# Optimization experiments

Measured on AMD Instinct MI355X. Metric: run time of the kernel, lower is better.

The kernel has to match this reference:

```python
import jax, jax.numpy as jnp
import numpy as np

C = 64   # in_channels
KS = 3   # kernel_size


def _wconv(p, W1, b1, W2, b2, W3, b3):
    # 1x1 conv stack: 3 -> 64 -> 256 -> C*KS*KS, ReLU between
    h = jax.nn.relu(jnp.einsum('oc,bchw->bohw', W1, p) + b1[None, :, None, None])
    h = jax.nn.relu(jnp.einsum('oc,bchw->bohw', W2, h) + b2[None, :, None, None])
    h = jnp.einsum('oc,bchw->bohw', W3, h) + b3[None, :, None, None]
    return h  # [1, C*KS*KS, ho, wo]


def setup_inputs() -> dict:
    key = jax.random.key(0)
    k = jax.random.split(key, 8)
    bs, hi, wi = 2, 128, 128
    ho, wo = 512, 512
    x = jax.random.normal(k[0], (bs, C, hi, wi), jnp.float32)
    poseMap = jax.random.normal(k[1], (1, 3, ho, wo), jnp.float32)
    interMapY = jax.random.randint(k[2], (ho, wo), 0, hi)
    interMapX = jax.random.randint(k[3], (ho, wo), 0, wi)
    W1 = jax.random.normal(k[4], (64, 3), jnp.float32) * 0.1
    b1 = jnp.zeros((64,), jnp.float32)
    W2 = jax.random.normal(k[5], (256, 64), jnp.float32) * 0.05
    b2 = jnp.zeros((256,), jnp.float32)
    W3 = jax.random.normal(k[6], (C * KS * KS, 256), jnp.float32) * 0.05
    b3 = jnp.zeros((C * KS * KS,), jnp.float32)
    return {'x': x, 'poseMap': poseMap, 'W1': W1, 'b1': b1, 'W2': W2, 'b2': b2,
            'W3': W3, 'b3': b3, 'interMapY': interMapY, 'interMapX': interMapX}


def reference(x, poseMap, W1, b1, W2, b2, W3, b3, interMapY, interMapX):
    bs, c, hi, wi = x.shape
    ho, wo = interMapY.shape
    # kernel prediction branch (poseMap is detached in the original)
    w = _wconv(jax.lax.stop_gradient(poseMap), W1, b1, W2, b2, W3, b3)
    w = w.reshape(C, KS * KS, ho, wo)
    sw = jax.nn.softmax(w, axis=1)  # softmax over the KS*KS taps
    # unfold(x, KS, padding=KS//2) tap k corresponds to xp[:, :, i + k//KS, j + k%KS]
    pad = KS // 2
    xp = jnp.pad(x, ((0, 0), (0, 0), (pad, pad), (pad, pad)))
    out = jnp.zeros((bs, C, ho, wo), x.dtype)
    for k in range(KS * KS):  # fixed small loop over taps; fuses gather+weight+reduce
        dy, dx = k // KS, k % KS
        g = xp[:, :, interMapY + dy, interMapX + dx]  # [bs, C, ho, wo] paired gather
        out = out + g * sw[None, :, k]  # sw[:, k] -> [C, ho, wo]
    return out
```

## Files before the change

### kernel.cpp

```cpp
#include <hip/hip_runtime.h>
#include <math.h>

#define HO 512
#define WO 512
#define HI 128
#define WI 128
#define CC 64
#define BS 2
#define NPX 64
#define NT 256

#define W2P_ELEMS (16 * 2 * 64 * 8)
#define W3P_ELEMS (36 * 8 * 64 * 8)
#define TOTALW    (W2P_ELEMS + W3P_ELEMS)
#define XT_ELEM_OFF TOTALW
#define NBORDER4  16512

typedef __attribute__((ext_vector_type(8))) short short8;
typedef __attribute__((ext_vector_type(4))) float float4v;
typedef __attribute__((ext_vector_type(2))) float float2v;

__device__ __forceinline__ unsigned short f2bf(float f) {
    unsigned u = __builtin_bit_cast(unsigned, f);
    unsigned r = (u + 0x7FFFu + ((u >> 16) & 1u)) >> 16;
    return (unsigned short)r;
}

__global__ void prepack_all(const float* __restrict__ x,
                            const float* __restrict__ W2,
                            const float* __restrict__ W3,
                            unsigned short* __restrict__ wsp,
                            float* __restrict__ xt) {
    const int tid = blockIdx.x * blockDim.x + threadIdx.x;
    if (tid < 262144) {
        const int pos = tid & 16383;
        const int g   = tid >> 14;
        const int h = pos >> 7, w = pos & 127;
        const float* src = x + pos;
        float a0[4], a1[4];
        #pragma unroll
        for (int j = 0; j < 4; ++j) a0[j] = src[(size_t)(g * 4 + j) * (HI * WI)];
        #pragma unroll
        for (int j = 0; j < 4; ++j) a1[j] = src[(size_t)(CC + g * 4 + j) * (HI * WI)];
        float* dst = xt + ((h + 1) * 130 + (w + 1)) * 128 + g * 8;
        *(float4v*)dst       = (float4v){a0[0], a1[0], a0[1], a1[1]};
        *(float4v*)(dst + 4) = (float4v){a0[2], a1[2], a0[3], a1[3]};
        return;
    }
    const int idx = tid - 262144;
    if (idx < W2P_ELEMS) {
        int j = idx & 7, lane = (idx >> 3) & 63, rest = idx >> 9;
        int ks = rest & 1, nt = rest >> 1;
        int n = nt * 16 + (lane & 15);
        int k = ks * 32 + (lane >> 4) * 8 + j;
        wsp[idx] = f2bf(W2[n * 64 + k]);
    } else if (idx < TOTALW) {
        int i2 = idx - W2P_ELEMS;
        int j = i2 & 7, lane = (i2 >> 3) & 63, rest = i2 >> 9;
        int ks = rest & 7, nt = rest >> 3;
        int tap = nt >> 2, ct = nt & 3;
        int row = (ct * 16 + (lane & 15)) * 9 + tap;
        int k = ks * 32 + (lane >> 4) * 8 + j;
        wsp[idx] = f2bf(W3[row * 256 + k]);
    } else if (idx < TOTALW + NBORDER4) {
        int a = idx - TOTALW;
        int cell;
        if (a < 2 * 130 * 32) {
            int r = a / (130 * 32);
            int rest = a - r * (130 * 32);
            cell = (r * 129) * 130 + (rest >> 5);
            a = rest;
        } else {
            int a2 = a - 2 * 130 * 32;
            int h = 1 + (a2 >> 6);
            int rest = a2 & 63;
            cell = h * 130 + (rest >> 5) * 129;
            a = rest;
        }
        float4v z = {0.f, 0.f, 0.f, 0.f};
        *(float4v*)(xt + (size_t)cell * 128 + (a & 31) * 4) = z;
    }
}

__global__ __launch_bounds__(NT, 3)
void fused_main(const float* __restrict__ xt, const float* __restrict__ pose,
                const float* __restrict__ W1, const float* __restrict__ b1,
                const float* __restrict__ b2, const float* __restrict__ b3,
                const int* __restrict__ iY, const int* __restrict__ iX,
                const unsigned short* __restrict__ wsp,
                float* __restrict__ out)
{
    __shared__ char smem[33792 + 768 + 512];
    unsigned short (*sH2)[264] = (unsigned short (*)[264])&smem[0];
    unsigned short (*sH1)[72]  = (unsigned short (*)[72])&smem[0];
    float (*sP)[NPX]           = (float (*)[NPX])&smem[33792];
    int* sIY                   = (int*)&smem[34560];
    int* sIX                   = (int*)&smem[34816];

    const int t = threadIdx.x;
    const int pixBase = blockIdx.x * NPX;
    const int y  = pixBase / WO;
    const int x0 = pixBase % WO;

    if (t < 192) sP[t >> 6][t & 63] = pose[(t >> 6) * (HO * WO) + pixBase + (t & 63)];
    if (t < 64) sIY[t] = iY[pixBase + t];
    else if (t < 128) sIX[t - 64] = iX[pixBase + t - 64];
    __syncthreads();

    {
        const int p  = t & 63;
        const int og = t >> 6;
        const float p0 = sP[0][p], p1 = sP[1][p], p2 = sP[2][p];
        #pragma unroll
        for (int i = 0; i < 16; i += 2) {
            const int o = og * 16 + i;
            float a0 = fmaf(W1[o * 3 + 2], p2, fmaf(W1[o * 3 + 1], p1, fmaf(W1[o * 3 + 0], p0, b1[o])));
            float a1 = fmaf(W1[o * 3 + 5], p2, fmaf(W1[o * 3 + 4], p1, fmaf(W1[o * 3 + 3], p0, b1[o + 1])));
            a0 = fmaxf(a0, 0.f); a1 = fmaxf(a1, 0.f);
            unsigned pack = (unsigned)f2bf(a0) | ((unsigned)f2bf(a1) << 16);
            *(unsigned*)&sH1[p][o] = pack;
        }
    }
    __syncthreads();

    const int wv = t >> 6, l = t & 63, lm = l & 15, lq = l >> 4;
    const int m0 = wv * 16;

    short8 a0 = *(const short8*)&sH1[m0 + lm][0  + lq * 8];
    short8 a1 = *(const short8*)&sH1[m0 + lm][32 + lq * 8];
    __syncthreads();

    {
        const short8* w2f = (const short8*)wsp;
        #pragma unroll 4
        for (int nt = 0; nt < 16; ++nt) {
            float4v acc = {0.f, 0.f, 0.f, 0.f};
            short8 bf0 = w2f[(nt * 2 + 0) * 64 + l];
            short8 bf1 = w2f[(nt * 2 + 1) * 64 + l];
            acc = __builtin_amdgcn_mfma_f32_16x16x32_bf16(a0, bf0, acc, 0, 0, 0);
            acc = __builtin_amdgcn_mfma_f32_16x16x32_bf16(a1, bf1, acc, 0, 0, 0);
            const float bv = b2[nt * 16 + lm];
            #pragma unroll
            for (int r = 0; r < 4; ++r)
                sH2[m0 + lq * 4 + r][nt * 16 + lm] = f2bf(fmaxf(acc[r] + bv, 0.f));
        }
    }

    int pbase[4];
    #pragma unroll
    for (int r = 0; r < 4; ++r) {
        const int p = m0 + lq * 4 + r;
        pbase[r] = ((sIY[p] + 1) * 130 + (sIX[p] + 1)) * 128;
    }
    const int koff[9] = {-131 * 128, -130 * 128, -129 * 128,
                         -1 * 128,   0,          1 * 128,
                         129 * 128,  130 * 128,  131 * 128};
    const short8* w3f = (const short8*)(wsp + W2P_ELEMS);

    for (int ct = 0; ct < 4; ++ct) {
        float4v accs[9];
        #pragma unroll
        for (int tap = 0; tap < 9; ++tap) accs[tap] = (float4v){0.f, 0.f, 0.f, 0.f};

        #pragma unroll 2
        for (int ks = 0; ks < 8; ++ks) {
            short8 a = *(const short8*)&sH2[m0 + lm][ks * 32 + lq * 8];
            #pragma unroll
            for (int tap = 0; tap < 9; ++tap) {
                short8 b = w3f[(((tap << 2) | ct) * 8 + ks) * 64 + l];
                accs[tap] = __builtin_amdgcn_mfma_f32_16x16x32_bf16(a, b, accs[tap], 0, 0, 0);
            }
        }

        const int c = ct * 16 + lm;
        float bv[9];
        #pragma unroll
        for (int tap = 0; tap < 9; ++tap) bv[tap] = b3[c * 9 + tap];

        float ob0[4], ob1[4];
        #pragma unroll
        for (int r = 0; r < 4; ++r) {
            float lg[9];
            #pragma unroll
            for (int tap = 0; tap < 9; ++tap) lg[tap] = accs[tap][r] + bv[tap];
            float mx = lg[0];
            #pragma unroll
            for (int tap = 1; tap < 9; ++tap) mx = fmaxf(mx, lg[tap]);
            const float* xb = xt + pbase[r] + 2 * c;
            float s = 0.f, o0 = 0.f, o1 = 0.f;
            #pragma unroll
            for (int tap = 0; tap < 9; ++tap) {
                const float ev = __expf(lg[tap] - mx);
                const float2v gg = *(const float2v*)(xb + koff[tap]);
                s += ev;
                o0 = fmaf(ev, gg[0], o0);
                o1 = fmaf(ev, gg[1], o1);
            }
            const float inv = 1.f / s;
            ob0[r] = o0 * inv;
            ob1[r] = o1 * inv;
        }

        const int px = x0 + m0 + lq * 4;
        float* op0 = out + ((size_t)c * HO + y) * WO + px;
        float* op1 = op0 + (size_t)CC * HO * WO;
        *(float4v*)op0 = (float4v){ob0[0], ob0[1], ob0[2], ob0[3]};
        *(float4v*)op1 = (float4v){ob1[0], ob1[1], ob1[2], ob1[3]};
    }
}

extern "C" void kernel_launch(void* const* d_in, const int* in_sizes, int n_in,
                              void* d_out, int out_size, void* d_ws, size_t ws_size,
                              hipStream_t stream) {
    const float* x    = (const float*)d_in[0];
    const float* pose = (const float*)d_in[1];
    const float* W1   = (const float*)d_in[2];
    const float* b1   = (const float*)d_in[3];
    const float* W2   = (const float*)d_in[4];
    const float* b2   = (const float*)d_in[5];
    const float* W3   = (const float*)d_in[6];
    const float* b3   = (const float*)d_in[7];
    const int*   iY   = (const int*)d_in[8];
    const int*   iX   = (const int*)d_in[9];
    float* out = (float*)d_out;
    unsigned short* wsp = (unsigned short*)d_ws;
    float* xt = (float*)((char*)d_ws + (size_t)XT_ELEM_OFF * sizeof(unsigned short));

    prepack_all<<<2048, NT, 0, stream>>>(x, W2, W3, wsp, xt);

    const int nblocks = (HO * WO) / NPX;
    fused_main<<<nblocks, NT, 0, stream>>>(
        xt, pose, W1, b1, b2, b3, iY, iX, wsp, out);
}
```

Measured before the change: 405.3 us.

## Switch third conv GEMM to 32x32x16 MFMA with per-wave channel-half tiling

Repacks W3 for the 32x32x16 bf16 MFMA and restructures the final GEMM so each wave computes a 32-pixel by 32-channel tile over all 9 taps in one pass, rather than looping over four 16-channel tiles with 16x16x32 MFMAs. The gather base offsets are precomputed once per pixel into shared memory. The aim is to raise MFMA throughput and cut redundant A-fragment reloads. In exchange it holds 144 accumulator registers per lane, so occupancy is lowered from 3 to 2 blocks per CU, with a risk of spills or less latency hiding for the gathers.

```diff
diff --git a/kernel.cpp b/kernel.cpp
--- a/kernel.cpp
+++ b/kernel.cpp
@@ -11,7 +11,7 @@
 #define NT 256
 
 #define W2P_ELEMS (16 * 2 * 64 * 8)
-#define W3P_ELEMS (36 * 8 * 64 * 8)
+#define W3P_ELEMS (18 * 16 * 64 * 8)
 #define TOTALW    (W2P_ELEMS + W3P_ELEMS)
 #define XT_ELEM_OFF TOTALW
 #define NBORDER4  16512
@@ -19,6 +19,7 @@
 typedef __attribute__((ext_vector_type(8))) short short8;
 typedef __attribute__((ext_vector_type(4))) float float4v;
 typedef __attribute__((ext_vector_type(2))) float float2v;
+typedef __attribute__((ext_vector_type(16))) float float16v;
 
 __device__ __forceinline__ unsigned short f2bf(float f) {
     unsigned u = __builtin_bit_cast(unsigned, f);
@@ -57,10 +58,11 @@
     } else if (idx < TOTALW) {
         int i2 = idx - W2P_ELEMS;
         int j = i2 & 7, lane = (i2 >> 3) & 63, rest = i2 >> 9;
-        int ks = rest & 7, nt = rest >> 3;
-        int tap = nt >> 2, ct = nt & 3;
-        int row = (ct * 16 + (lane & 15)) * 9 + tap;
-        int k = ks * 32 + (lane >> 4) * 8 + j;
+        int ks = rest & 15, rest2 = rest >> 4;
+        int tap = rest2 % 9, half = rest2 / 9;
+        int ch = half * 32 + (lane & 31);
+        int row = ch * 9 + tap;
+        int k = ks * 16 + (lane >> 5) * 8 + j;
         wsp[idx] = f2bf(W3[row * 256 + k]);
     } else if (idx < TOTALW + NBORDER4) {
         int a = idx - TOTALW;
@@ -82,7 +84,7 @@
     }
 }
 
-__global__ __launch_bounds__(NT, 3)
+__global__ __launch_bounds__(NT, 2)
 void fused_main(const float* __restrict__ xt, const float* __restrict__ pose,
                 const float* __restrict__ W1, const float* __restrict__ b1,
                 const float* __restrict__ b2, const float* __restrict__ b3,
@@ -90,12 +92,11 @@
                 const unsigned short* __restrict__ wsp,
                 float* __restrict__ out)
 {
-    __shared__ char smem[33792 + 768 + 512];
+    __shared__ char smem[33792 + 768 + 256];
     unsigned short (*sH2)[264] = (unsigned short (*)[264])&smem[0];
     unsigned short (*sH1)[72]  = (unsigned short (*)[72])&smem[0];
     float (*sP)[NPX]           = (float (*)[NPX])&smem[33792];
-    int* sIY                   = (int*)&smem[34560];
-    int* sIX                   = (int*)&smem[34816];
+    int* sPB                   = (int*)&smem[34560];
 
     const int t = threadIdx.x;
     const int pixBase = blockIdx.x * NPX;
@@ -103,8 +104,7 @@
     const int x0 = pixBase % WO;
 
     if (t < 192) sP[t >> 6][t & 63] = pose[(t >> 6) * (HO * WO) + pixBase + (t & 63)];
-    if (t < 64) sIY[t] = iY[pixBase + t];
-    else if (t < 128) sIX[t - 64] = iX[pixBase + t - 64];
+    if (t < 64)  sPB[t] = ((iY[pixBase + t] + 1) * 130 + (iX[pixBase + t] + 1)) * 128;
     __syncthreads();
 
     {
@@ -145,48 +145,54 @@
                 sH2[m0 + lq * 4 + r][nt * 16 + lm] = f2bf(fmaxf(acc[r] + bv, 0.f));
         }
     }
-
-    int pbase[4];
-    #pragma unroll
-    for (int r = 0; r < 4; ++r) {
-        const int p = m0 + lq * 4 + r;
-        pbase[r] = ((sIY[p] + 1) * 130 + (sIX[p] + 1)) * 128;
-    }
+    __syncthreads();
+
+    const int hi  = l >> 5;
+    const int ln  = l & 31;
+    const int m0p = (wv >> 1) * 32;
+    const int chh = wv & 1;
+    const int c   = chh * 32 + ln;
+
+    const short8* w3f = (const short8*)(wsp + W2P_ELEMS);
+
+    float16v accs[9];
+    #pragma unroll
+    for (int tap = 0; tap < 9; ++tap)
+        accs[tap] = (float16v)(0.f);
+
+    #pragma unroll
+    for (int ks = 0; ks < 16; ++ks) {
+        short8 a = *(const short8*)&sH2[m0p + ln][ks * 16 + hi * 8];
+        #pragma unroll
+        for (int tap = 0; tap < 9; ++tap) {
+            short8 b = w3f[(((chh * 9) + tap) * 16 + ks) * 64 + l];
+            accs[tap] = __builtin_amdgcn_mfma_f32_32x32x16_bf16(a, b, accs[tap], 0, 0, 0);
+        }
+    }
+
+    float bv[9];
+    #pragma unroll
+    for (int tap = 0; tap < 9; ++tap) bv[tap] = b3[c * 9 + tap];
+
     const int koff[9] = {-131 * 128, -130 * 128, -129 * 128,
                          -1 * 128,   0,          1 * 128,
                          129 * 128,  130 * 128,  131 * 128};
-    const short8* w3f = (const short8*)(wsp + W2P_ELEMS);
-
-    for (int ct = 0; ct < 4; ++ct) {
-        float4v accs[9];
-        #pragma unroll
-        for (int tap = 0; tap < 9; ++tap) accs[tap] = (float4v){0.f, 0.f, 0.f, 0.f};
-
-        #pragma unroll 2
-        for (int ks = 0; ks < 8; ++ks) {
-            short8 a = *(const short8*)&sH2[m0 + lm][ks * 32 + lq * 8];
-            #pragma unroll
-            for (int tap = 0; tap < 9; ++tap) {
-                short8 b = w3f[(((tap << 2) | ct) * 8 + ks) * 64 + l];
-                accs[tap] = __builtin_amdgcn_mfma_f32_16x16x32_bf16(a, b, accs[tap], 0, 0, 0);
-            }
-        }
-
-        const int c = ct * 16 + lm;
-        float bv[9];
-        #pragma unroll
-        for (int tap = 0; tap < 9; ++tap) bv[tap] = b3[c * 9 + tap];
-
+
+    #pragma unroll
+    for (int rq = 0; rq < 4; ++rq) {
         float ob0[4], ob1[4];
         #pragma unroll
-        for (int r = 0; r < 4; ++r) {
+        for (int ri = 0; ri < 4; ++ri) {
+            const int r = rq * 4 + ri;
+            const int pxl = m0p + ri + 8 * rq + 4 * hi;
+            const int pb = sPB[pxl];
             float lg[9];
             #pragma unroll
             for (int tap = 0; tap < 9; ++tap) lg[tap] = accs[tap][r] + bv[tap];
             float mx = lg[0];
             #pragma unroll
             for (int tap = 1; tap < 9; ++tap) mx = fmaxf(mx, lg[tap]);
-            const float* xb = xt + pbase[r] + 2 * c;
+            const float* xb = xt + pb + 2 * c;
             float s = 0.f, o0 = 0.f, o1 = 0.f;
             #pragma unroll
             for (int tap = 0; tap < 9; ++tap) {
@@ -197,11 +203,10 @@
                 o1 = fmaf(ev, gg[1], o1);
             }
             const float inv = 1.f / s;
-            ob0[r] = o0 * inv;
-            ob1[r] = o1 * inv;
-        }
-
-        const int px = x0 + m0 + lq * 4;
+            ob0[ri] = o0 * inv;
+            ob1[ri] = o1 * inv;
+        }
+        const int px = x0 + m0p + 8 * rq + 4 * hi;
         float* op0 = out + ((size_t)c * HO + y) * WO + px;
         float* op1 = op0 + (size_t)CC * HO * WO;
         *(float4v*)op0 = (float4v){ob0[0], ob0[1], ob0[2], ob0[3]};
```

Result: slower. 551.4 us (+36.0%).
